# Kernel tuning notes

Measured on AMD Instinct MI355X. Metric: run time of the kernel, lower is better.

Reference implementation:

```python
import jax, jax.numpy as jnp
import numpy as np

B, T, C, H = 4, 2048, 2048, 16
HD = C // H  # head_dim = 128


def setup_inputs() -> dict:
    key = jax.random.key(0)
    k1, k2, k3 = jax.random.split(key, 3)
    x = jax.random.normal(k1, (B, T, C), dtype=jnp.float32)
    w_qkv = jax.random.normal(k2, (C, 3 * C), dtype=jnp.float32) * (C ** -0.5)
    w_proj = jax.random.normal(k3, (C, C), dtype=jnp.float32) * (C ** -0.5)
    return {"x": x, "w_qkv": w_qkv, "w_proj": w_proj}


def reference(x, w_qkv, w_proj):
    Bx, Tx, Cx = x.shape
    qkv = x @ w_qkv                       # [B, T, 3C]
    q, k, v = jnp.split(qkv, 3, axis=-1)  # each [B, T, C]

    def split_heads(t):
        return t.reshape(Bx, Tx, H, HD).transpose(0, 2, 1, 3)  # [B, H, T, HD]

    q, k, v = split_heads(q), split_heads(k), split_heads(v)
    scale = HD ** -0.5
    attn = jnp.einsum("bhqd,bhkd->bhqk", q, k) * scale  # [B, H, T, T]
    causal = jnp.tril(jnp.ones((Tx, Tx), dtype=bool))
    attn = jnp.where(causal[None, None], attn, -jnp.inf)
    attn = jax.nn.softmax(attn, axis=-1)
    out = jnp.einsum("bhqk,bhkd->bhqd", attn, v)        # [B, H, T, HD]
    out = out.transpose(0, 2, 1, 3).reshape(Bx, Tx, Cx)  # [B, T, C]
    return out @ w_proj
```

## Files before the change

### kernel.cpp

```cpp
#include <hip/hip_runtime.h>
#include <hip/hip_bf16.h>
#include <math.h>

typedef __bf16 bf16;
typedef __bf16 bf16x8 __attribute__((ext_vector_type(8)));
typedef float f32x4 __attribute__((ext_vector_type(4)));

#define AS1(p) ((const __attribute__((address_space(1))) void*)(p))
#define AS3(p) ((__attribute__((address_space(3))) void*)(p))

__device__ __forceinline__ void gl_lds16(const bf16* g, bf16* l) {
    __builtin_amdgcn_global_load_lds(AS1(g), AS3(l), 16, 0, 0);
}

__global__ __launch_bounds__(256) void cast_f32_bf16(const float* __restrict__ in,
                                                     bf16* __restrict__ out, long n) {
    long i = ((long)blockIdx.x * 256 + threadIdx.x) * 4;
    if (i + 3 < n) {
        float4 v = *(const float4*)(in + i);
        out[i + 0] = (bf16)v.x;
        out[i + 1] = (bf16)v.y;
        out[i + 2] = (bf16)v.z;
        out[i + 3] = (bf16)v.w;
    }
}

__global__ __launch_bounds__(256) void transpose_cast(const float* __restrict__ in,
                                                      bf16* __restrict__ out,
                                                      int R, int Cc) {
    __shared__ float tile[32][33];
    const int t = threadIdx.x;
    const int r0 = blockIdx.y * 32, c0 = blockIdx.x * 32;
    for (int i = 0; i < 4; ++i) {
        int idx = t + i * 256;
        int r = idx >> 5, c = idx & 31;
        tile[r][c] = in[(size_t)(r0 + r) * Cc + c0 + c];
    }
    __syncthreads();
    for (int i = 0; i < 4; ++i) {
        int idx = t + i * 256;
        int r = idx >> 5, c = idx & 31;
        out[(size_t)(c0 + r) * R + r0 + c] = (bf16)tile[c][r];
    }
}

template <typename OT>
__global__ __launch_bounds__(256, 4) void gemm_bt(const bf16* __restrict__ A,
                                                  const bf16* __restrict__ BT,
                                                  OT* __restrict__ C,
                                                  int M, int N, int K) {
    __shared__ bf16 lA[128 * 64];
    __shared__ bf16 lB[128 * 64];
    const int t = threadIdx.x;
    const int lane = t & 63;
    const int w = t >> 6;
    const int wr = w >> 1, wc = w & 1;
    const int l15 = lane & 15, lg = lane >> 4;

    const int nbx = gridDim.x, nby = gridDim.y;
    const int orig = blockIdx.y * nbx + blockIdx.x;
    const int span = nby * 8;
    const int grp = orig / span, rem = orig % span;
    const int bm = rem >> 3, bn = grp * 8 + (rem & 7);

    const bf16* Abase = A + (size_t)bm * 128 * K;
    const bf16* Bbase = BT + (size_t)bn * 128 * K;

    f32x4 acc[4][4] = {};

    for (int k0 = 0; k0 < K; k0 += 64) {
        for (int j = 0; j < 4; ++j) {
            int cid = j * 256 + t;
            int r = cid >> 3, c = cid & 7;
            int src = (c ^ (r & 7)) << 3;
            gl_lds16(Abase + (size_t)r * K + k0 + src, lA + (size_t)cid * 8);
            gl_lds16(Bbase + (size_t)r * K + k0 + src, lB + (size_t)cid * 8);
        }
        __syncthreads();
        bf16x8 af[2][4], bfr[2][4];
        for (int kk = 0; kk < 2; ++kk) {
            for (int m = 0; m < 4; ++m) {
                int R = wr * 64 + m * 16 + l15;
                af[kk][m] = *(const bf16x8*)(lA + R * 64 + (((kk * 4 + lg) ^ (R & 7)) << 3));
            }
            for (int n = 0; n < 4; ++n) {
                int R = wc * 64 + n * 16 + l15;
                bfr[kk][n] = *(const bf16x8*)(lB + R * 64 + (((kk * 4 + lg) ^ (R & 7)) << 3));
            }
        }
        for (int kk = 0; kk < 2; ++kk)
            for (int m = 0; m < 4; ++m)
                for (int n = 0; n < 4; ++n)
                    acc[m][n] = __builtin_amdgcn_mfma_f32_16x16x32_bf16(af[kk][m], bfr[kk][n], acc[m][n], 0, 0, 0);
        __syncthreads();
    }

    for (int m = 0; m < 4; ++m)
        for (int n = 0; n < 4; ++n) {
            int row = bm * 128 + wr * 64 + m * 16 + lg * 4;
            int col = bn * 128 + wc * 64 + n * 16 + l15;
            for (int r = 0; r < 4; ++r)
                C[(size_t)(row + r) * N + col] = (OT)acc[m][n][r];
        }
}

__global__ __launch_bounds__(256, 2) void attn_fwd(const bf16* __restrict__ QKV,
                                                   bf16* __restrict__ O) {
    __shared__ bf16 lK[64 * 128];
    __shared__ bf16 lVt[128 * 64];
    __shared__ bf16 lP[4][32 * 68];

    const int t = threadIdx.x, lane = t & 63, w = t >> 6;
    const int l15 = lane & 15, lg = lane >> 4;
    const int bh = blockIdx.y;
    const int b = bh >> 4, h = bh & 15;
    const size_t rs = 6144;

    const bf16* Qb = QKV + (size_t)b * 2048 * rs + h * 128;
    const bf16* Kb = Qb + 2048;
    const bf16* Vb = Qb + 4096;

    const float C = 0.12751705f;
    const int kvp = t & 31;
    const int hd0 = (t >> 5) * 16;

    for (int half = 0; half < 2; ++half) {
        const int qt = half == 0 ? (15 - (int)blockIdx.x) : (int)blockIdx.x;
        const int q0 = qt * 128;
        const int qa = q0 + w * 32;

        bf16x8 qf[2][4];
        for (int f = 0; f < 2; ++f)
            for (int kk = 0; kk < 4; ++kk)
                qf[f][kk] = *(const bf16x8*)(Qb + (size_t)(qa + f * 16 + l15) * rs + kk * 32 + lg * 8);

        f32x4 o[2][8] = {};
        float m2[2][4], l2[2][4];
        for (int f = 0; f < 2; ++f)
            for (int r = 0; r < 4; ++r) { m2[f][r] = -1e30f; l2[f][r] = 0.f; }

        const int nt = q0 / 64 + 2;

        for (int j = 0; j < 4; ++j) {
            int c = j * 256 + t;
            int r = c >> 4, cc = c & 15;
            gl_lds16(Kb + (size_t)r * rs + ((cc ^ (r & 7)) << 3), lK + (size_t)c * 8);
        }
        bf16x8 vr0, vr1, vr2, vr3;
        {
            const bf16* p = Vb + (size_t)(2 * kvp) * rs + hd0;
            vr0 = *(const bf16x8*)(p);
            vr1 = *(const bf16x8*)(p + rs);
            vr2 = *(const bf16x8*)(p + 8);
            vr3 = *(const bf16x8*)(p + rs + 8);
        }

        for (int kt = 0; kt < nt; ++kt) {
            const int kv0 = kt * 64;
            __syncthreads();

            for (int e = 0; e < 8; ++e) {
                union { bf16 h2[2]; unsigned u; } p0, p1;
                p0.h2[0] = vr0[e]; p0.h2[1] = vr1[e];
                p1.h2[0] = vr2[e]; p1.h2[1] = vr3[e];
                int r0 = hd0 + e, r1 = hd0 + 8 + e;
                *(unsigned*)(lVt + r0 * 64 + (((kvp >> 2) ^ (r0 & 7)) << 3) + ((kvp & 3) << 1)) = p0.u;
                *(unsigned*)(lVt + r1 * 64 + (((kvp >> 2) ^ (r1 & 7)) << 3) + ((kvp & 3) << 1)) = p1.u;
            }

            f32x4 s[2][4] = {};
            __builtin_amdgcn_s_setprio(1);
            for (int n = 0; n < 4; ++n) {
                int row = n * 16 + l15;
                for (int kk = 0; kk < 4; ++kk) {
                    bf16x8 kf = *(const bf16x8*)(lK + row * 128 + (((kk * 4 + lg) ^ (row & 7)) << 3));
                    s[0][n] = __builtin_amdgcn_mfma_f32_16x16x32_bf16(qf[0][kk], kf, s[0][n], 0, 0, 0);
                    s[1][n] = __builtin_amdgcn_mfma_f32_16x16x32_bf16(qf[1][kk], kf, s[1][n], 0, 0, 0);
                }
            }
            __builtin_amdgcn_s_setprio(0);

            float pv[2][4][4];
            for (int f = 0; f < 2; ++f)
                for (int n = 0; n < 4; ++n)
                    for (int r = 0; r < 4; ++r) {
                        float x = s[f][n][r] * C;
                        int qg = qa + f * 16 + lg * 4 + r;
                        int kg = kv0 + n * 16 + l15;
                        pv[f][n][r] = (kg <= qg) ? x : -1e30f;
                    }
            float pmax[2][4];
            for (int f = 0; f < 2; ++f)
                for (int r = 0; r < 4; ++r)
                    pmax[f][r] = fmaxf(fmaxf(pv[f][0][r], pv[f][1][r]), fmaxf(pv[f][2][r], pv[f][3][r]));
            for (int d = 1; d < 16; d <<= 1)
                for (int f = 0; f < 2; ++f)
                    for (int r = 0; r < 4; ++r)
                        pmax[f][r] = fmaxf(pmax[f][r], __shfl_xor(pmax[f][r], d));
            bool need = false;
            for (int f = 0; f < 2; ++f)
                for (int r = 0; r < 4; ++r)
                    need = need || (pmax[f][r] > m2[f][r] + 8.f);
            if (__any(need ? 1 : 0)) {
                for (int f = 0; f < 2; ++f)
                    for (int r = 0; r < 4; ++r) {
                        float mn = fmaxf(m2[f][r], pmax[f][r]);
                        float al = exp2f(m2[f][r] - mn);
                        m2[f][r] = mn;
                        l2[f][r] *= al;
                        for (int j = 0; j < 8; ++j) o[f][j][r] *= al;
                    }
            }
            for (int f = 0; f < 2; ++f)
                for (int n = 0; n < 4; ++n)
                    for (int r = 0; r < 4; ++r) {
                        float p = exp2f(pv[f][n][r] - m2[f][r]);
                        l2[f][r] += p;
                        lP[w][(f * 16 + lg * 4 + r) * 68 + n * 16 + l15] = (bf16)p;
                    }
            bf16x8 pf[2][2];
            for (int f = 0; f < 2; ++f) {
                pf[f][0] = *(const bf16x8*)(&lP[w][(f * 16 + l15) * 68 + lg * 8]);
                pf[f][1] = *(const bf16x8*)(&lP[w][(f * 16 + l15) * 68 + 32 + lg * 8]);
            }

            __syncthreads();

            if (kt + 1 < nt) {
                const int nk = kv0 + 64;
                for (int j = 0; j < 4; ++j) {
                    int c = j * 256 + t;
                    int r = c >> 4, cc = c & 15;
                    gl_lds16(Kb + (size_t)(nk + r) * rs + ((cc ^ (r & 7)) << 3), lK + (size_t)c * 8);
                }
                const bf16* p = Vb + (size_t)(nk + 2 * kvp) * rs + hd0;
                vr0 = *(const bf16x8*)(p);
                vr1 = *(const bf16x8*)(p + rs);
                vr2 = *(const bf16x8*)(p + 8);
                vr3 = *(const bf16x8*)(p + rs + 8);
            }

            __builtin_amdgcn_s_setprio(1);
            for (int j = 0; j < 8; ++j) {
                int R = j * 16 + l15;
                bf16x8 vfa = *(const bf16x8*)(lVt + R * 64 + ((lg ^ (R & 7)) << 3));
                bf16x8 vfb = *(const bf16x8*)(lVt + R * 64 + (((4 + lg) ^ (R & 7)) << 3));
                o[0][j] = __builtin_amdgcn_mfma_f32_16x16x32_bf16(pf[0][0], vfa, o[0][j], 0, 0, 0);
                o[0][j] = __builtin_amdgcn_mfma_f32_16x16x32_bf16(pf[0][1], vfb, o[0][j], 0, 0, 0);
                o[1][j] = __builtin_amdgcn_mfma_f32_16x16x32_bf16(pf[1][0], vfa, o[1][j], 0, 0, 0);
                o[1][j] = __builtin_amdgcn_mfma_f32_16x16x32_bf16(pf[1][1], vfb, o[1][j], 0, 0, 0);
            }
            __builtin_amdgcn_s_setprio(0);
        }

        for (int d = 1; d < 16; d <<= 1)
            for (int f = 0; f < 2; ++f)
                for (int r = 0; r < 4; ++r)
                    l2[f][r] += __shfl_xor(l2[f][r], d);
        for (int f = 0; f < 2; ++f) {
            float inv[4];
            for (int r = 0; r < 4; ++r) inv[r] = 1.f / l2[f][r];
            bf16* Ob = O + ((size_t)b * 2048 + qa + f * 16) * 2048 + h * 128;
            for (int j = 0; j < 8; ++j)
                for (int r = 0; r < 4; ++r)
                    Ob[(size_t)(lg * 4 + r) * 2048 + j * 16 + l15] = (bf16)(o[f][j][r] * inv[r]);
        }
    }
}

extern "C" void kernel_launch(void* const* d_in, const int* in_sizes, int n_in,
                              void* d_out, int out_size, void* d_ws, size_t ws_size,
                              hipStream_t stream) {
    const float* x     = (const float*)d_in[0];
    const float* wqkv  = (const float*)d_in[1];
    const float* wproj = (const float*)d_in[2];
    float* out = (float*)d_out;

    char* ws = (char*)d_ws;
    bf16* xb     = (bf16*)(ws);
    bf16* wqkvT  = (bf16*)(ws + 33554432);
    bf16* wprojT = (bf16*)(ws + 33554432 + 25165824);
    bf16* QKV    = (bf16*)(ws + 33554432 + 25165824 + 8388608);
    bf16* Obuf   = xb;

    cast_f32_bf16<<<dim3(16384), 256, 0, stream>>>(x, xb, (long)8192 * 2048);
    transpose_cast<<<dim3(192, 64), 256, 0, stream>>>(wqkv, wqkvT, 2048, 6144);
    transpose_cast<<<dim3(64, 64), 256, 0, stream>>>(wproj, wprojT, 2048, 2048);
    gemm_bt<bf16><<<dim3(48, 64), 256, 0, stream>>>(xb, wqkvT, QKV, 8192, 6144, 2048);
    attn_fwd<<<dim3(8, 64), 256, 0, stream>>>(QKV, Obuf);
    gemm_bt<float><<<dim3(16, 64), 256, 0, stream>>>(Obuf, wprojT, out, 8192, 2048, 2048);
}
```

Measured before the change: 547.6 us.

## Use 256x256 double-buffered GEMM tiles with 512-thread blocks

Result: faster. 459.7 us (-16.1%).

```diff
diff --git a/kernel.cpp b/kernel.cpp
--- a/kernel.cpp
+++ b/kernel.cpp
@@ -45,16 +45,15 @@
 }
 
 template <typename OT>
-__global__ __launch_bounds__(256, 4) void gemm_bt(const bf16* __restrict__ A,
-                                                  const bf16* __restrict__ BT,
-                                                  OT* __restrict__ C,
-                                                  int M, int N, int K) {
-    __shared__ bf16 lA[128 * 64];
-    __shared__ bf16 lB[128 * 64];
+__global__ __launch_bounds__(512, 2) void gemm256_bt(const bf16* __restrict__ A,
+                                                     const bf16* __restrict__ BT,
+                                                     OT* __restrict__ C,
+                                                     int M, int N, int K) {
+    __shared__ bf16 lds[2][2][256 * 64];
     const int t = threadIdx.x;
     const int lane = t & 63;
     const int w = t >> 6;
-    const int wr = w >> 1, wc = w & 1;
+    const int wr = w >> 2, wc = w & 3;
     const int l15 = lane & 15, lg = lane >> 4;
 
     const int nbx = gridDim.x, nby = gridDim.y;
@@ -63,42 +62,61 @@
     const int grp = orig / span, rem = orig % span;
     const int bm = rem >> 3, bn = grp * 8 + (rem & 7);
 
-    const bf16* Abase = A + (size_t)bm * 128 * K;
-    const bf16* Bbase = BT + (size_t)bn * 128 * K;
-
-    f32x4 acc[4][4] = {};
-
-    for (int k0 = 0; k0 < K; k0 += 64) {
-        for (int j = 0; j < 4; ++j) {
-            int cid = j * 256 + t;
-            int r = cid >> 3, c = cid & 7;
-            int src = (c ^ (r & 7)) << 3;
-            gl_lds16(Abase + (size_t)r * K + k0 + src, lA + (size_t)cid * 8);
-            gl_lds16(Bbase + (size_t)r * K + k0 + src, lB + (size_t)cid * 8);
-        }
+    const bf16* Ab = A + (size_t)bm * 256 * K;
+    const bf16* Bb = BT + (size_t)bn * 256 * K;
+
+    f32x4 acc[8][4] = {};
+
+    const int nk = K / 64;
+    int cur = 0;
+    for (int j = 0; j < 4; ++j) {
+        int cid = j * 512 + t;
+        int r = cid >> 3, c = cid & 7;
+        int src = (c ^ (r & 7)) << 3;
+        gl_lds16(Ab + (size_t)r * K + src, &lds[0][0][cid * 8]);
+        gl_lds16(Bb + (size_t)r * K + src, &lds[0][1][cid * 8]);
+    }
+
+    for (int kt = 0; kt < nk; ++kt) {
         __syncthreads();
-        bf16x8 af[2][4], bfr[2][4];
-        for (int kk = 0; kk < 2; ++kk) {
-            for (int m = 0; m < 4; ++m) {
-                int R = wr * 64 + m * 16 + l15;
-                af[kk][m] = *(const bf16x8*)(lA + R * 64 + (((kk * 4 + lg) ^ (R & 7)) << 3));
-            }
+
+        if (kt + 1 < nk) {
+            const int k0 = (kt + 1) * 64;
+            for (int j = 0; j < 4; ++j) {
+                int cid = j * 512 + t;
+                int r = cid >> 3, c = cid & 7;
+                int src = (c ^ (r & 7)) << 3;
+                gl_lds16(Ab + (size_t)r * K + k0 + src, &lds[cur ^ 1][0][cid * 8]);
+                gl_lds16(Bb + (size_t)r * K + k0 + src, &lds[cur ^ 1][1][cid * 8]);
+            }
+        }
+
+        const bf16* lA = &lds[cur][0][0];
+        const bf16* lB = &lds[cur][1][0];
+        bf16x8 bfrag[2][4];
+        for (int kk = 0; kk < 2; ++kk)
             for (int n = 0; n < 4; ++n) {
                 int R = wc * 64 + n * 16 + l15;
-                bfr[kk][n] = *(const bf16x8*)(lB + R * 64 + (((kk * 4 + lg) ^ (R & 7)) << 3));
-            }
-        }
-        for (int kk = 0; kk < 2; ++kk)
-            for (int m = 0; m < 4; ++m)
-                for (int n = 0; n < 4; ++n)
-                    acc[m][n] = __builtin_amdgcn_mfma_f32_16x16x32_bf16(af[kk][m], bfr[kk][n], acc[m][n], 0, 0, 0);
-        __syncthreads();
-    }
-
-    for (int m = 0; m < 4; ++m)
+                bfrag[kk][n] = *(const bf16x8*)(lB + R * 64 + (((kk * 4 + lg) ^ (R & 7)) << 3));
+            }
+        __builtin_amdgcn_s_setprio(1);
+        for (int m = 0; m < 8; ++m) {
+            int R = wr * 128 + m * 16 + l15;
+            bf16x8 a0 = *(const bf16x8*)(lA + R * 64 + ((lg ^ (R & 7)) << 3));
+            bf16x8 a1 = *(const bf16x8*)(lA + R * 64 + (((4 + lg) ^ (R & 7)) << 3));
+            for (int n = 0; n < 4; ++n) {
+                acc[m][n] = __builtin_amdgcn_mfma_f32_16x16x32_bf16(a0, bfrag[0][n], acc[m][n], 0, 0, 0);
+                acc[m][n] = __builtin_amdgcn_mfma_f32_16x16x32_bf16(a1, bfrag[1][n], acc[m][n], 0, 0, 0);
+            }
+        }
+        __builtin_amdgcn_s_setprio(0);
+        cur ^= 1;
+    }
+
+    for (int m = 0; m < 8; ++m)
         for (int n = 0; n < 4; ++n) {
-            int row = bm * 128 + wr * 64 + m * 16 + lg * 4;
-            int col = bn * 128 + wc * 64 + n * 16 + l15;
+            int row = bm * 256 + wr * 128 + m * 16 + lg * 4;
+            int col = bn * 256 + wc * 64 + n * 16 + l15;
             for (int r = 0; r < 4; ++r)
                 C[(size_t)(row + r) * N + col] = (OT)acc[m][n][r];
         }
@@ -227,13 +245,13 @@
             __syncthreads();
 
             if (kt + 1 < nt) {
-                const int nk = kv0 + 64;
+                const int nk2 = kv0 + 64;
                 for (int j = 0; j < 4; ++j) {
                     int c = j * 256 + t;
                     int r = c >> 4, cc = c & 15;
-                    gl_lds16(Kb + (size_t)(nk + r) * rs + ((cc ^ (r & 7)) << 3), lK + (size_t)c * 8);
+                    gl_lds16(Kb + (size_t)(nk2 + r) * rs + ((cc ^ (r & 7)) << 3), lK + (size_t)c * 8);
                 }
-                const bf16* p = Vb + (size_t)(nk + 2 * kvp) * rs + hd0;
+                const bf16* p = Vb + (size_t)(nk2 + 2 * kvp) * rs + hd0;
                 vr0 = *(const bf16x8*)(p);
                 vr1 = *(const bf16x8*)(p + rs);
                 vr2 = *(const bf16x8*)(p + 8);
@@ -286,7 +304,7 @@
     cast_f32_bf16<<<dim3(16384), 256, 0, stream>>>(x, xb, (long)8192 * 2048);
     transpose_cast<<<dim3(192, 64), 256, 0, stream>>>(wqkv, wqkvT, 2048, 6144);
     transpose_cast<<<dim3(64, 64), 256, 0, stream>>>(wproj, wprojT, 2048, 2048);
-    gemm_bt<bf16><<<dim3(48, 64), 256, 0, stream>>>(xb, wqkvT, QKV, 8192, 6144, 2048);
+    gemm256_bt<bf16><<<dim3(24, 32), 512, 0, stream>>>(xb, wqkvT, QKV, 8192, 6144, 2048);
     attn_fwd<<<dim3(8, 64), 256, 0, stream>>>(QKV, Obuf);
-    gemm_bt<float><<<dim3(16, 64), 256, 0, stream>>>(Obuf, wprojT, out, 8192, 2048, 2048);
-}
+    gemm256_bt<float><<<dim3(8, 32), 512, 0, stream>>>(Obuf, wprojT, out, 8192, 2048, 2048);
+}
```
